# Performance work log

Hardware: AMD Instinct MI355X
Metric: run time of the kernel (lower is better)

## Reference

```python
import jax, jax.numpy as jnp
import numpy as np

NEG_BIG = -9e15
ALPHA = 0.2  # leakyrelu slope

N, IN_F, OUT_F = 8192, 512, 64


def setup_inputs() -> dict:
    key = jax.random.key(0)
    ks = jax.random.split(key, 7)
    return {
        "input": jax.random.normal(ks[0], (N, IN_F), dtype=jnp.float32),
        "W": jax.random.normal(ks[1], (IN_F, OUT_F), dtype=jnp.float32) * 0.05,
        "a": jax.random.normal(ks[2], (2 * OUT_F, 1), dtype=jnp.float32) * 0.1,
        "W_si": jax.random.normal(ks[3], (1, 1), dtype=jnp.float32),
        "W_ei": jax.random.normal(ks[4], (1, 1), dtype=jnp.float32),
        "adj_ad": jax.random.uniform(ks[5], (N, N), dtype=jnp.float32),
        "adj": jax.random.randint(ks[6], (N, N), 0, 2, dtype=jnp.int32),
    }


def reference(input, W, a, W_si, W_ei, adj_ad, adj):
    h = input @ W                                   # [N, F]
    F_ = h.shape[1]
    a1, a2 = a[:F_, 0], a[F_:, 0]                   # split concat projection
    # concat-score: a^T [h_i || h_j] == (h@a1)_i + (h@a2)_j, no [N,N,2F] tensor
    e = jax.nn.leaky_relu(h @ a1[:, None] + (h @ a2[:, None]).T, ALPHA)  # [N, N]
    e = jnp.abs(W_ei) * e + jnp.abs(W_si) * adj_ad
    attention = jnp.where(adj > 0, e, jnp.float32(NEG_BIG))
    attention = jax.nn.softmax(attention, axis=1)
    # dropout is identity in eval mode (training=False)
    h_prime = attention @ h                         # [N, F]
    return jax.nn.elu(h_prime)
```

## Files before the change

kernel.cpp:

```cpp
#include <hip/hip_runtime.h>
#include <math.h>

#define N 8192
#define IN_F 512
#define OUTF 64
#define TI 16
#define JT 256
#define NTILE (N / JT)
#define PS 264

typedef _Float16 f16x8 __attribute__((ext_vector_type(8)));
typedef float f32x4 __attribute__((ext_vector_type(4)));

#define OFF_HT   0u
#define OFF_S    262144u
#define OFF_T    270336u
#define OFF_TMAX 278528u

#define SB0() __builtin_amdgcn_sched_barrier(0)
#define SYNC()                                           \
  SB0();                                                 \
  asm volatile("s_waitcnt lgkmcnt(0)" ::: "memory");     \
  SB0();                                                 \
  __builtin_amdgcn_s_barrier();                          \
  SB0();

__device__ __forceinline__ unsigned enc_f32(float f) {
  unsigned b = __float_as_uint(f);
  return b ^ ((unsigned)((int)b >> 31) | 0x80000000u);
}

__global__ __launch_bounds__(64) void k_precompute(
    const float* __restrict__ input, const float* __restrict__ W,
    const float* __restrict__ a, const float* __restrict__ W_ei,
    _Float16* __restrict__ hT, float* __restrict__ s2,
    float* __restrict__ t2) {
  const int lane = threadIdx.x;
  const int i0 = blockIdx.x * 4;
  const float aei = fabsf(W_ei[0]);

  float acc[4] = {0.f, 0.f, 0.f, 0.f};
  for (int c = 0; c < IN_F; c += 4) {
    const float w0 = W[(c + 0) * OUTF + lane];
    const float w1 = W[(c + 1) * OUTF + lane];
    const float w2 = W[(c + 2) * OUTF + lane];
    const float w3 = W[(c + 3) * OUTF + lane];
    #pragma unroll
    for (int r = 0; r < 4; r++) {
      const float4 iv = *(const float4*)(input + (size_t)(i0 + r) * IN_F + c);
      acc[r] += iv.x * w0 + iv.y * w1 + iv.z * w2 + iv.w * w3;
    }
  }

  union { _Float16 f[4]; uint2 u; } pk;
  #pragma unroll
  for (int r = 0; r < 4; r++) pk.f[r] = (_Float16)acc[r];
  *(uint2*)(hT + (size_t)lane * N + i0) = pk.u;

  const float a1v = a[lane];
  const float a2v = a[OUTF + lane];
  #pragma unroll
  for (int r = 0; r < 4; r++) {
    float sv = acc[r] * a1v;
    float tv = acc[r] * a2v;
    #pragma unroll
    for (int off = 1; off < 64; off <<= 1) {
      sv += __shfl_xor(sv, off);
      tv += __shfl_xor(tv, off);
    }
    if (lane == 0) {
      s2[i0 + r] = aei * sv;
      t2[i0 + r] = aei * tv;
    }
  }
}

__global__ __launch_bounds__(512) void k_tmax(const float* __restrict__ t,
                                              unsigned* __restrict__ tmax) {
  __shared__ float red[8];
  const int tid = threadIdx.x;
  float m = t[blockIdx.x * 512 + tid];
  #pragma unroll
  for (int off = 1; off < 64; off <<= 1) m = fmaxf(m, __shfl_xor(m, off));
  if ((tid & 63) == 0) red[tid >> 6] = m;
  __syncthreads();
  if (tid == 0) {
    #pragma unroll
    for (int w = 1; w < 8; w++) m = fmaxf(m, red[w]);
    atomicMax(tmax, enc_f32(m));
  }
}

__global__ __launch_bounds__(512, 4) void k_attn(
    const _Float16* __restrict__ hT, const float* __restrict__ s2,
    const float* __restrict__ t2, const unsigned* __restrict__ tmaxp,
    const float* __restrict__ W_si, const float* __restrict__ W_ei,
    const float* __restrict__ adj_ad, const int* __restrict__ adj,
    float* __restrict__ out) {
  __shared__ __align__(16) float smem[8224];
  _Float16* P = (_Float16*)smem;

  const int tid = threadIdx.x;
  const int w = tid >> 6;
  const int lane = tid & 63;
  const int q = lane >> 4;
  const int m = lane & 15;
  const int h2 = lane >> 5;
  const int cw = lane & 31;
  const int i0 = blockIdx.x * TI;

  const float asi = fabsf(W_si[0]);
  (void)W_ei;
  const unsigned te = *tmaxp;
  const float tm2 = __uint_as_float((te & 0x80000000u) ? (te ^ 0x80000000u) : ~te);

  const int myrow = 2 * w + h2;
  const float s2r = s2[i0 + myrow];
  const float ym = s2r + tm2;
  const float MrB = fmaxf(ym, 0.2f * ym) + asi;

  float S = 0.f;
  f32x4 acc[4];
  #pragma unroll
  for (int nb = 0; nb < 4; nb++) acc[nb] = (f32x4){0.f, 0.f, 0.f, 0.f};

  const size_t gRow = (size_t)(i0 + myrow) * N;
  const int c0 = cw * 4;

  struct PF { float4 a0, a1; int4 k0, k1; };

  auto LOADT = [&](int kt) -> PF {
    const size_t b = gRow + (size_t)kt * JT + c0;
    PF p;
    p.a0 = *(const float4*)(adj_ad + b);
    p.a1 = *(const float4*)(adj_ad + b + 128);
    p.k0 = *(const int4*)(adj + b);
    p.k1 = *(const int4*)(adj + b + 128);
    return p;
  };

  auto EXPW = [&](int kt, const PF& p, const float4& tva, const float4& tvb) {
    const float ad[8] = {p.a0.x, p.a0.y, p.a0.z, p.a0.w,
                         p.a1.x, p.a1.y, p.a1.z, p.a1.w};
    const int mk[8] = {p.k0.x, p.k0.y, p.k0.z, p.k0.w,
                       p.k1.x, p.k1.y, p.k1.z, p.k1.w};
    const float tv[8] = {tva.x, tva.y, tva.z, tva.w,
                         tvb.x, tvb.y, tvb.z, tvb.w};
    union { _Float16 hh[8]; uint2 u[2]; } pk;
    #pragma unroll
    for (int e = 0; e < 8; e++) {
      const float y = s2r + tv[e];
      const float lr = fmaxf(y, 0.2f * y);
      const float arg = fmaf(asi, ad[e], lr - MrB);
      const float pv = __expf(arg) * (float)mk[e];
      S += pv;
      pk.hh[e] = (_Float16)pv;
    }
    _Float16* dst = P + (kt & 1) * (16 * PS) + myrow * PS;
    *(uint2*)(dst + c0) = pk.u[0];
    *(uint2*)(dst + c0 + 128) = pk.u[1];
  };

  #define MLOAD(kt, FB, FA)                                                   \
    {                                                                         \
      const int cb_ = (kt) * JT + w * 32 + q * 8;                             \
      _Pragma("unroll") for (int nb = 0; nb < 4; nb++)                        \
          FB[nb] = *(const f16x8*)(hT + (size_t)(nb * 16 + m) * N + cb_);     \
      FA = *(const f16x8*)(P + ((kt) & 1) * (16 * PS) + m * PS + w * 32 +     \
                           q * 8);                                            \
    }

  #define MSTEP(FB, FA)                                                       \
    {                                                                         \
      _Pragma("unroll") for (int nb = 0; nb < 4; nb++)                        \
          acc[nb] = __builtin_amdgcn_mfma_f32_16x16x32_f16(FA, FB[nb],        \
                                                           acc[nb], 0, 0, 0);\
    }

  PF pA = LOADT(0);
  PF pB;

  #pragma unroll 1
  for (int k = 0; k < NTILE; k += 2) {
    {
      const float4 tva = *(const float4*)(t2 + k * JT + c0);
      const float4 tvb = *(const float4*)(t2 + k * JT + c0 + 128);
      f16x8 fb[4], fa;
      if (k >= 1) MLOAD(k - 1, fb, fa);
      SB0();
      pB = LOADT(k + 1);
      SB0();
      if (k >= 1) MSTEP(fb, fa);
      EXPW(k, pA, tva, tvb);
      SYNC();
    }
    {
      const float4 tva = *(const float4*)(t2 + (k + 1) * JT + c0);
      const float4 tvb = *(const float4*)(t2 + (k + 1) * JT + c0 + 128);
      f16x8 fb[4], fa;
      MLOAD(k, fb, fa);
      SB0();
      if (k + 2 < NTILE) pA = LOADT(k + 2);
      SB0();
      MSTEP(fb, fa);
      EXPW(k + 1, pB, tva, tvb);
      SYNC();
    }
  }

  {
    f16x8 fb[4], fa;
    MLOAD(NTILE - 1, fb, fa);
    MSTEP(fb, fa);
  }

  #pragma unroll
  for (int off = 1; off < 32; off <<= 1) S += __shfl_xor(S, off);

  SYNC();

  if ((lane & 31) == 0) smem[8192 + myrow] = S;
  #pragma unroll
  for (int nb = 0; nb < 4; nb++) {
    #pragma unroll
    for (int reg = 0; reg < 4; reg++) {
      smem[w * 1024 + (q * 4 + reg) * 64 + nb * 16 + m] = acc[nb][reg];
    }
  }
  __syncthreads();

  #pragma unroll
  for (int ii = 0; ii < 2; ii++) {
    const int e = tid + 512 * ii;
    const int r = e >> 6;
    const int f = e & 63;
    float num = 0.f;
    #pragma unroll
    for (int ww = 0; ww < 8; ww++) num += smem[ww * 1024 + r * 64 + f];
    const float den = smem[8192 + r];
    const float x = num / den;
    out[(size_t)(i0 + r) * OUTF + f] = x > 0.f ? x : expm1f(x);
  }
}

extern "C" void kernel_launch(void* const* d_in, const int* in_sizes, int n_in,
                              void* d_out, int out_size, void* d_ws, size_t ws_size,
                              hipStream_t stream) {
  const float* input  = (const float*)d_in[0];
  const float* W      = (const float*)d_in[1];
  const float* a      = (const float*)d_in[2];
  const float* W_si   = (const float*)d_in[3];
  const float* W_ei   = (const float*)d_in[4];
  const float* adj_ad = (const float*)d_in[5];
  const int*   adj    = (const int*)d_in[6];
  float* out = (float*)d_out;
  float* ws  = (float*)d_ws;

  _Float16* hT   = (_Float16*)(ws + OFF_HT);
  float* s2      = ws + OFF_S;
  float* t2      = ws + OFF_T;
  unsigned* tmax = (unsigned*)(ws + OFF_TMAX);

  hipMemsetAsync(tmax, 0, 4, stream);
  k_precompute<<<N / 4, 64, 0, stream>>>(input, W, a, W_ei, hT, s2, t2);
  k_tmax<<<N / 512, 512, 0, stream>>>(t2, tmax);
  k_attn<<<N / TI, 512, 0, stream>>>(hT, s2, t2, tmax, W_si, W_ei,
                                     adj_ad, adj, out);
}
```

Baseline: 578.4 us.

## Pack adjacency into bitmask in precompute kernel and fuse tmax reduction

The precompute kernel now streams the int32 adjacency matrix once and packs it into a one-bit-per-entry mask. The attention kernel then reads a single mask byte per 8 columns instead of two int4 loads, which cuts its load pressure and register use. The separate tmax kernel is folded into precompute through a per-block atomicMax. The per-lane column mapping changes to 8 contiguous columns so the P tile is written with one 16-byte store. Total adj traffic is unchanged but moves into the small, lightly occupied precompute kernel, with an extra 8MB mask written and read back.

```diff
diff --git a/kernel.cpp b/kernel.cpp
--- a/kernel.cpp
+++ b/kernel.cpp
@@ -8,14 +8,17 @@
 #define JT 256
 #define NTILE (N / JT)
 #define PS 264
+#define MROW 1024
 
 typedef _Float16 f16x8 __attribute__((ext_vector_type(8)));
 typedef float f32x4 __attribute__((ext_vector_type(4)));
+typedef int i32x4 __attribute__((ext_vector_type(4)));
 
 #define OFF_HT   0u
 #define OFF_S    262144u
 #define OFF_T    270336u
 #define OFF_TMAX 278528u
+#define OFF_MASK 294912u
 
 #define SB0() __builtin_amdgcn_sched_barrier(0)
 #define SYNC()                                           \
@@ -33,70 +36,91 @@
 __global__ __launch_bounds__(64) void k_precompute(
     const float* __restrict__ input, const float* __restrict__ W,
     const float* __restrict__ a, const float* __restrict__ W_ei,
-    _Float16* __restrict__ hT, float* __restrict__ s2,
-    float* __restrict__ t2) {
+    const int* __restrict__ adj, _Float16* __restrict__ hT,
+    float* __restrict__ s2, float* __restrict__ t2,
+    unsigned* __restrict__ tmax, unsigned char* __restrict__ mask) {
   const int lane = threadIdx.x;
   const int i0 = blockIdx.x * 4;
   const float aei = fabsf(W_ei[0]);
 
-  float acc[4] = {0.f, 0.f, 0.f, 0.f};
-  for (int c = 0; c < IN_F; c += 4) {
-    const float w0 = W[(c + 0) * OUTF + lane];
-    const float w1 = W[(c + 1) * OUTF + lane];
-    const float w2 = W[(c + 2) * OUTF + lane];
-    const float w3 = W[(c + 3) * OUTF + lane];
+  auto GEMM = [&]() {
+    float acc[4] = {0.f, 0.f, 0.f, 0.f};
+    for (int c = 0; c < IN_F; c += 4) {
+      const float w0 = W[(c + 0) * OUTF + lane];
+      const float w1 = W[(c + 1) * OUTF + lane];
+      const float w2 = W[(c + 2) * OUTF + lane];
+      const float w3 = W[(c + 3) * OUTF + lane];
+      #pragma unroll
+      for (int r = 0; r < 4; r++) {
+        const float4 iv = *(const float4*)(input + (size_t)(i0 + r) * IN_F + c);
+        acc[r] += iv.x * w0 + iv.y * w1 + iv.z * w2 + iv.w * w3;
+      }
+    }
+
+    union { _Float16 f[4]; uint2 u; } pk;
+    #pragma unroll
+    for (int r = 0; r < 4; r++) pk.f[r] = (_Float16)acc[r];
+    *(uint2*)(hT + (size_t)lane * N + i0) = pk.u;
+
+    const float a1v = a[lane];
+    const float a2v = a[OUTF + lane];
+    float tloc = -1e30f;
     #pragma unroll
     for (int r = 0; r < 4; r++) {
-      const float4 iv = *(const float4*)(input + (size_t)(i0 + r) * IN_F + c);
-      acc[r] += iv.x * w0 + iv.y * w1 + iv.z * w2 + iv.w * w3;
-    }
-  }
-
-  union { _Float16 f[4]; uint2 u; } pk;
-  #pragma unroll
-  for (int r = 0; r < 4; r++) pk.f[r] = (_Float16)acc[r];
-  *(uint2*)(hT + (size_t)lane * N + i0) = pk.u;
-
-  const float a1v = a[lane];
-  const float a2v = a[OUTF + lane];
-  #pragma unroll
-  for (int r = 0; r < 4; r++) {
-    float sv = acc[r] * a1v;
-    float tv = acc[r] * a2v;
-    #pragma unroll
-    for (int off = 1; off < 64; off <<= 1) {
-      sv += __shfl_xor(sv, off);
-      tv += __shfl_xor(tv, off);
-    }
-    if (lane == 0) {
-      s2[i0 + r] = aei * sv;
-      t2[i0 + r] = aei * tv;
-    }
-  }
-}
-
-__global__ __launch_bounds__(512) void k_tmax(const float* __restrict__ t,
-                                              unsigned* __restrict__ tmax) {
-  __shared__ float red[8];
-  const int tid = threadIdx.x;
-  float m = t[blockIdx.x * 512 + tid];
-  #pragma unroll
-  for (int off = 1; off < 64; off <<= 1) m = fmaxf(m, __shfl_xor(m, off));
-  if ((tid & 63) == 0) red[tid >> 6] = m;
-  __syncthreads();
-  if (tid == 0) {
-    #pragma unroll
-    for (int w = 1; w < 8; w++) m = fmaxf(m, red[w]);
-    atomicMax(tmax, enc_f32(m));
-  }
+      float sv = acc[r] * a1v;
+      float tv = acc[r] * a2v;
+      #pragma unroll
+      for (int off = 1; off < 64; off <<= 1) {
+        sv += __shfl_xor(sv, off);
+        tv += __shfl_xor(tv, off);
+      }
+      if (lane == 0) {
+        s2[i0 + r] = aei * sv;
+        const float t2v = aei * tv;
+        t2[i0 + r] = t2v;
+        tloc = fmaxf(tloc, t2v);
+      }
+    }
+    if (lane == 0) atomicMax(tmax, enc_f32(tloc));
+  };
+
+  auto MASK = [&]() {
+    const unsigned gtid = blockIdx.x * 64 + lane;
+    #pragma unroll 1
+    for (int o = 0; o < 64; o += 4) {
+      i32x4 v[4][2];
+      #pragma unroll
+      for (int u = 0; u < 4; u++) {
+        const size_t B = gtid + (size_t)(o + u) * 131072;
+        const i32x4* p = (const i32x4*)adj + B * 2;
+        v[u][0] = __builtin_nontemporal_load(p);
+        v[u][1] = __builtin_nontemporal_load(p + 1);
+      }
+      #pragma unroll
+      for (int u = 0; u < 4; u++) {
+        const size_t B = gtid + (size_t)(o + u) * 131072;
+        const unsigned b = (unsigned)(v[u][0].x > 0) |
+                           ((unsigned)(v[u][0].y > 0) << 1) |
+                           ((unsigned)(v[u][0].z > 0) << 2) |
+                           ((unsigned)(v[u][0].w > 0) << 3) |
+                           ((unsigned)(v[u][1].x > 0) << 4) |
+                           ((unsigned)(v[u][1].y > 0) << 5) |
+                           ((unsigned)(v[u][1].z > 0) << 6) |
+                           ((unsigned)(v[u][1].w > 0) << 7);
+        mask[B] = (unsigned char)b;
+      }
+    }
+  };
+
+  if (blockIdx.x & 1) { MASK(); GEMM(); }
+  else                { GEMM(); MASK(); }
 }
 
 __global__ __launch_bounds__(512, 4) void k_attn(
     const _Float16* __restrict__ hT, const float* __restrict__ s2,
     const float* __restrict__ t2, const unsigned* __restrict__ tmaxp,
-    const float* __restrict__ W_si, const float* __restrict__ W_ei,
-    const float* __restrict__ adj_ad, const int* __restrict__ adj,
-    float* __restrict__ out) {
+    const float* __restrict__ W_si, const unsigned char* __restrict__ mask,
+    const float* __restrict__ adj_ad, float* __restrict__ out) {
   __shared__ __align__(16) float smem[8224];
   _Float16* P = (_Float16*)smem;
 
@@ -110,7 +134,6 @@
   const int i0 = blockIdx.x * TI;
 
   const float asi = fabsf(W_si[0]);
-  (void)W_ei;
   const unsigned te = *tmaxp;
   const float tm2 = __uint_as_float((te & 0x80000000u) ? (te ^ 0x80000000u) : ~te);
 
@@ -125,40 +148,37 @@
   for (int nb = 0; nb < 4; nb++) acc[nb] = (f32x4){0.f, 0.f, 0.f, 0.f};
 
   const size_t gRow = (size_t)(i0 + myrow) * N;
-  const int c0 = cw * 4;
-
-  struct PF { float4 a0, a1; int4 k0, k1; };
+  const unsigned char* mrow = mask + (size_t)(i0 + myrow) * MROW;
+  const int c0 = cw * 8;
+
+  struct PF { float4 a0, a1; unsigned mb; };
 
   auto LOADT = [&](int kt) -> PF {
     const size_t b = gRow + (size_t)kt * JT + c0;
     PF p;
     p.a0 = *(const float4*)(adj_ad + b);
-    p.a1 = *(const float4*)(adj_ad + b + 128);
-    p.k0 = *(const int4*)(adj + b);
-    p.k1 = *(const int4*)(adj + b + 128);
+    p.a1 = *(const float4*)(adj_ad + b + 4);
+    p.mb = mrow[kt * 32 + cw];
     return p;
   };
 
   auto EXPW = [&](int kt, const PF& p, const float4& tva, const float4& tvb) {
     const float ad[8] = {p.a0.x, p.a0.y, p.a0.z, p.a0.w,
                          p.a1.x, p.a1.y, p.a1.z, p.a1.w};
-    const int mk[8] = {p.k0.x, p.k0.y, p.k0.z, p.k0.w,
-                       p.k1.x, p.k1.y, p.k1.z, p.k1.w};
     const float tv[8] = {tva.x, tva.y, tva.z, tva.w,
                          tvb.x, tvb.y, tvb.z, tvb.w};
-    union { _Float16 hh[8]; uint2 u[2]; } pk;
+    union { _Float16 hh[8]; uint4 u4; } pk;
     #pragma unroll
     for (int e = 0; e < 8; e++) {
       const float y = s2r + tv[e];
       const float lr = fmaxf(y, 0.2f * y);
       const float arg = fmaf(asi, ad[e], lr - MrB);
-      const float pv = __expf(arg) * (float)mk[e];
+      const float pv = ((p.mb >> e) & 1u) ? __expf(arg) : 0.f;
       S += pv;
       pk.hh[e] = (_Float16)pv;
     }
     _Float16* dst = P + (kt & 1) * (16 * PS) + myrow * PS;
-    *(uint2*)(dst + c0) = pk.u[0];
-    *(uint2*)(dst + c0 + 128) = pk.u[1];
+    *(uint4*)(dst + c0) = pk.u4;
   };
 
   #define MLOAD(kt, FB, FA)                                                   \
@@ -184,7 +204,7 @@
   for (int k = 0; k < NTILE; k += 2) {
     {
       const float4 tva = *(const float4*)(t2 + k * JT + c0);
-      const float4 tvb = *(const float4*)(t2 + k * JT + c0 + 128);
+      const float4 tvb = *(const float4*)(t2 + k * JT + c0 + 4);
       f16x8 fb[4], fa;
       if (k >= 1) MLOAD(k - 1, fb, fa);
       SB0();
@@ -196,7 +216,7 @@
     }
     {
       const float4 tva = *(const float4*)(t2 + (k + 1) * JT + c0);
-      const float4 tvb = *(const float4*)(t2 + (k + 1) * JT + c0 + 128);
+      const float4 tvb = *(const float4*)(t2 + (k + 1) * JT + c0 + 4);
       f16x8 fb[4], fa;
       MLOAD(k, fb, fa);
       SB0();
@@ -256,14 +276,15 @@
   float* out = (float*)d_out;
   float* ws  = (float*)d_ws;
 
-  _Float16* hT   = (_Float16*)(ws + OFF_HT);
-  float* s2      = ws + OFF_S;
-  float* t2      = ws + OFF_T;
-  unsigned* tmax = (unsigned*)(ws + OFF_TMAX);
+  _Float16* hT        = (_Float16*)(ws + OFF_HT);
+  float* s2           = ws + OFF_S;
+  float* t2           = ws + OFF_T;
+  unsigned* tmax      = (unsigned*)(ws + OFF_TMAX);
+  unsigned char* mask = (unsigned char*)(ws + OFF_MASK);
 
   hipMemsetAsync(tmax, 0, 4, stream);
-  k_precompute<<<N / 4, 64, 0, stream>>>(input, W, a, W_ei, hT, s2, t2);
-  k_tmax<<<N / 512, 512, 0, stream>>>(t2, tmax);
-  k_attn<<<N / TI, 512, 0, stream>>>(hT, s2, t2, tmax, W_si, W_ei,
-                                     adj_ad, adj, out);
-}
+  k_precompute<<<N / 4, 64, 0, stream>>>(input, W, a, W_ei, adj, hT, s2, t2,
+                                         tmax, mask);
+  k_attn<<<N / TI, 512, 0, stream>>>(hT, s2, t2, tmax, W_si, mask,
+                                     adj_ad, out);
+}
```

After: 588.2 us. Within noise of the previous version (+1.7%).

## Split attention over column chunks with single-wave blocks and a finish kernel

Applied to the files above, without the earlier changes.

Restructures the attention kernel so each single-wavefront block handles 16 rows over one eighth of the columns. This removes the cross-wave LDS barriers and the in-block reduction, and partial numerators and denominators go to workspace. A new finish kernel sums the partials and applies normalization and ELU. The tmax reduction is folded into the precompute kernel via an atomic, which drops one launch. The cost is more partial-result traffic, an extra kernel, and hT fragments reloaded from global memory per block.

```diff
diff --git a/kernel.cpp b/kernel.cpp
--- a/kernel.cpp
+++ b/kernel.cpp
@@ -5,9 +5,11 @@
 #define IN_F 512
 #define OUTF 64
 #define TI 16
-#define JT 256
-#define NTILE (N / JT)
-#define PS 264
+#define JSPLIT 8
+#define JCH (N / JSPLIT)
+#define JT 64
+#define NT (JCH / JT)
+#define PS 72
 
 typedef _Float16 f16x8 __attribute__((ext_vector_type(8)));
 typedef float f32x4 __attribute__((ext_vector_type(4)));
@@ -16,14 +18,10 @@
 #define OFF_S    262144u
 #define OFF_T    270336u
 #define OFF_TMAX 278528u
+#define OFF_DEN  294912u
+#define OFF_NUM  360448u
 
 #define SB0() __builtin_amdgcn_sched_barrier(0)
-#define SYNC()                                           \
-  SB0();                                                 \
-  asm volatile("s_waitcnt lgkmcnt(0)" ::: "memory");     \
-  SB0();                                                 \
-  __builtin_amdgcn_s_barrier();                          \
-  SB0();
 
 __device__ __forceinline__ unsigned enc_f32(float f) {
   unsigned b = __float_as_uint(f);
@@ -34,7 +32,7 @@
     const float* __restrict__ input, const float* __restrict__ W,
     const float* __restrict__ a, const float* __restrict__ W_ei,
     _Float16* __restrict__ hT, float* __restrict__ s2,
-    float* __restrict__ t2) {
+    float* __restrict__ t2, unsigned* __restrict__ tmax) {
   const int lane = threadIdx.x;
   const int i0 = blockIdx.x * 4;
   const float aei = fabsf(W_ei[0]);
@@ -59,6 +57,7 @@
 
   const float a1v = a[lane];
   const float a2v = a[OUTF + lane];
+  float tloc = -1e30f;
   #pragma unroll
   for (int r = 0; r < 4; r++) {
     float sv = acc[r] * a1v;
@@ -70,177 +69,160 @@
     }
     if (lane == 0) {
       s2[i0 + r] = aei * sv;
-      t2[i0 + r] = aei * tv;
-    }
-  }
-}
-
-__global__ __launch_bounds__(512) void k_tmax(const float* __restrict__ t,
-                                              unsigned* __restrict__ tmax) {
-  __shared__ float red[8];
-  const int tid = threadIdx.x;
-  float m = t[blockIdx.x * 512 + tid];
-  #pragma unroll
-  for (int off = 1; off < 64; off <<= 1) m = fmaxf(m, __shfl_xor(m, off));
-  if ((tid & 63) == 0) red[tid >> 6] = m;
-  __syncthreads();
-  if (tid == 0) {
-    #pragma unroll
-    for (int w = 1; w < 8; w++) m = fmaxf(m, red[w]);
-    atomicMax(tmax, enc_f32(m));
-  }
-}
-
-__global__ __launch_bounds__(512, 4) void k_attn(
+      const float t2v = aei * tv;
+      t2[i0 + r] = t2v;
+      tloc = fmaxf(tloc, t2v);
+    }
+  }
+  if (lane == 0) atomicMax(tmax, enc_f32(tloc));
+}
+
+__global__ __launch_bounds__(64, 3) void k_attn(
     const _Float16* __restrict__ hT, const float* __restrict__ s2,
     const float* __restrict__ t2, const unsigned* __restrict__ tmaxp,
-    const float* __restrict__ W_si, const float* __restrict__ W_ei,
+    const float* __restrict__ W_si,
     const float* __restrict__ adj_ad, const int* __restrict__ adj,
-    float* __restrict__ out) {
-  __shared__ __align__(16) float smem[8224];
-  _Float16* P = (_Float16*)smem;
-
-  const int tid = threadIdx.x;
-  const int w = tid >> 6;
-  const int lane = tid & 63;
-  const int q = lane >> 4;
-  const int m = lane & 15;
-  const int h2 = lane >> 5;
-  const int cw = lane & 31;
-  const int i0 = blockIdx.x * TI;
+    float* __restrict__ numP, float* __restrict__ denP) {
+  __shared__ __align__(16) _Float16 P0[TI * PS];
+  __shared__ __align__(16) _Float16 P1[TI * PS];
+
+  const int lane = threadIdx.x;
+  const int g = lane >> 4;
+  const int cl = lane & 15;
+  const int ib = blockIdx.x >> 3;
+  const int js = blockIdx.x & 7;
+  const int i0 = ib * TI;
+  const int jb0 = js * JCH;
 
   const float asi = fabsf(W_si[0]);
-  (void)W_ei;
   const unsigned te = *tmaxp;
   const float tm2 = __uint_as_float((te & 0x80000000u) ? (te ^ 0x80000000u) : ~te);
 
-  const int myrow = 2 * w + h2;
-  const float s2r = s2[i0 + myrow];
-  const float ym = s2r + tm2;
-  const float MrB = fmaxf(ym, 0.2f * ym) + asi;
-
-  float S = 0.f;
+  float s2r[4], MrB[4];
+  #pragma unroll
+  for (int u = 0; u < 4; u++) {
+    s2r[u] = s2[i0 + 4 * u + g];
+    const float ym = s2r[u] + tm2;
+    MrB[u] = fmaxf(ym, 0.2f * ym) + asi;
+  }
+
+  float S[4] = {0.f, 0.f, 0.f, 0.f};
   f32x4 acc[4];
   #pragma unroll
   for (int nb = 0; nb < 4; nb++) acc[nb] = (f32x4){0.f, 0.f, 0.f, 0.f};
 
-  const size_t gRow = (size_t)(i0 + myrow) * N;
-  const int c0 = cw * 4;
-
-  struct PF { float4 a0, a1; int4 k0, k1; };
-
-  auto LOADT = [&](int kt) -> PF {
-    const size_t b = gRow + (size_t)kt * JT + c0;
-    PF p;
-    p.a0 = *(const float4*)(adj_ad + b);
-    p.a1 = *(const float4*)(adj_ad + b + 128);
-    p.k0 = *(const int4*)(adj + b);
-    p.k1 = *(const int4*)(adj + b + 128);
-    return p;
-  };
-
-  auto EXPW = [&](int kt, const PF& p, const float4& tva, const float4& tvb) {
-    const float ad[8] = {p.a0.x, p.a0.y, p.a0.z, p.a0.w,
-                         p.a1.x, p.a1.y, p.a1.z, p.a1.w};
-    const int mk[8] = {p.k0.x, p.k0.y, p.k0.z, p.k0.w,
-                       p.k1.x, p.k1.y, p.k1.z, p.k1.w};
-    const float tv[8] = {tva.x, tva.y, tva.z, tva.w,
-                         tvb.x, tvb.y, tvb.z, tvb.w};
-    union { _Float16 hh[8]; uint2 u[2]; } pk;
-    #pragma unroll
-    for (int e = 0; e < 8; e++) {
-      const float y = s2r + tv[e];
-      const float lr = fmaxf(y, 0.2f * y);
-      const float arg = fmaf(asi, ad[e], lr - MrB);
-      const float pv = __expf(arg) * (float)mk[e];
-      S += pv;
-      pk.hh[e] = (_Float16)pv;
-    }
-    _Float16* dst = P + (kt & 1) * (16 * PS) + myrow * PS;
-    *(uint2*)(dst + c0) = pk.u[0];
-    *(uint2*)(dst + c0 + 128) = pk.u[1];
-  };
-
-  #define MLOAD(kt, FB, FA)                                                   \
-    {                                                                         \
-      const int cb_ = (kt) * JT + w * 32 + q * 8;                             \
-      _Pragma("unroll") for (int nb = 0; nb < 4; nb++)                        \
-          FB[nb] = *(const f16x8*)(hT + (size_t)(nb * 16 + m) * N + cb_);     \
-      FA = *(const f16x8*)(P + ((kt) & 1) * (16 * PS) + m * PS + w * 32 +     \
-                           q * 8);                                            \
-    }
-
-  #define MSTEP(FB, FA)                                                       \
-    {                                                                         \
-      _Pragma("unroll") for (int nb = 0; nb < 4; nb++)                        \
-          acc[nb] = __builtin_amdgcn_mfma_f32_16x16x32_f16(FA, FB[nb],        \
-                                                           acc[nb], 0, 0, 0);\
-    }
-
-  PF pA = LOADT(0);
-  PF pB;
+  float4 vaA[4], vaB[4];
+  int4 vkA[4], vkB[4];
+
+  #define LOADS(kt, va, vk)                                                   \
+    {                                                                         \
+      const int cb_ = jb0 + (kt) * JT + cl * 4;                               \
+      _Pragma("unroll") for (int u = 0; u < 4; u++) {                         \
+        const size_t a_ = (size_t)(i0 + 4 * u + g) * N + cb_;                 \
+        va[u] = *(const float4*)(adj_ad + a_);                                \
+        vk[u] = *(const int4*)(adj + a_);                                     \
+      }                                                                       \
+    }
+
+  #define FBLOAD(kt, fb, t2v)                                                 \
+    {                                                                         \
+      const int jb_ = jb0 + (kt) * JT;                                        \
+      t2v = *(const float4*)(t2 + jb_ + cl * 4);                              \
+      _Pragma("unroll") for (int ks = 0; ks < 2; ks++)                        \
+        _Pragma("unroll") for (int nb = 0; nb < 4; nb++)                      \
+            fb[ks][nb] = *(const f16x8*)(hT + (size_t)(nb * 16 + cl) * N +    \
+                                         jb_ + ks * 32 + g * 8);              \
+    }
+
+  #define EXPW(va, vk, t2v, Pd)                                               \
+    {                                                                         \
+      const float tv_[4] = {t2v.x, t2v.y, t2v.z, t2v.w};                      \
+      _Pragma("unroll") for (int u = 0; u < 4; u++) {                         \
+        const float ad_[4] = {va[u].x, va[u].y, va[u].z, va[u].w};            \
+        const int mk_[4] = {vk[u].x, vk[u].y, vk[u].z, vk[u].w};              \
+        union { _Float16 h[4]; uint2 u2; } pk_;                               \
+        _Pragma("unroll") for (int e2 = 0; e2 < 4; e2++) {                    \
+          const float y_ = s2r[u] + tv_[e2];                                  \
+          const float lr_ = fmaxf(y_, 0.2f * y_);                             \
+          const float arg_ = fmaf(asi, ad_[e2], lr_ - MrB[u]);      \
+          const float pv_ = (mk_[e2] > 0) ? __expf(arg_) : 0.f;               \
+          S[u] += pv_;                                                        \
+          pk_.h[e2] = (_Float16)pv_;                                          \
+        }                                                                     \
+        *(uint2*)(Pd + (4 * u + g) * PS + cl * 4) = pk_.u2;                   \
+      }                                                                       \
+    }
+
+  #define MFMA4(Ps, fb)                                                       \
+    {                                                                         \
+      _Pragma("unroll") for (int ks = 0; ks < 2; ks++) {                      \
+        const f16x8 fa_ = *(const f16x8*)(Ps + cl * PS + ks * 32 + g * 8);    \
+        _Pragma("unroll") for (int nb = 0; nb < 4; nb++)                      \
+            acc[nb] = __builtin_amdgcn_mfma_f32_16x16x32_f16(                 \
+                fa_, fb[ks][nb], acc[nb], 0, 0, 0);                           \
+      }                                                                       \
+    }
+
+  LOADS(0, vaA, vkA);
+  SB0();
 
   #pragma unroll 1
-  for (int k = 0; k < NTILE; k += 2) {
+  for (int it = 0; it < NT / 2; it++) {
+    const int kt = 2 * it;
     {
-      const float4 tva = *(const float4*)(t2 + k * JT + c0);
-      const float4 tvb = *(const float4*)(t2 + k * JT + c0 + 128);
-      f16x8 fb[4], fa;
-      if (k >= 1) MLOAD(k - 1, fb, fa);
-      SB0();
-      pB = LOADT(k + 1);
-      SB0();
-      if (k >= 1) MSTEP(fb, fa);
-      EXPW(k, pA, tva, tvb);
-      SYNC();
+      f16x8 fb[2][4];
+      float4 t2v;
+      FBLOAD(kt, fb, t2v);
+      SB0();
+      LOADS(kt + 1, vaB, vkB);
+      SB0();
+      EXPW(vaA, vkA, t2v, P0);
+      MFMA4(P0, fb);
     }
     {
-      const float4 tva = *(const float4*)(t2 + (k + 1) * JT + c0);
-      const float4 tvb = *(const float4*)(t2 + (k + 1) * JT + c0 + 128);
-      f16x8 fb[4], fa;
-      MLOAD(k, fb, fa);
-      SB0();
-      if (k + 2 < NTILE) pA = LOADT(k + 2);
-      SB0();
-      MSTEP(fb, fa);
-      EXPW(k + 1, pB, tva, tvb);
-      SYNC();
-    }
-  }
-
-  {
-    f16x8 fb[4], fa;
-    MLOAD(NTILE - 1, fb, fa);
-    MSTEP(fb, fa);
-  }
-
-  #pragma unroll
-  for (int off = 1; off < 32; off <<= 1) S += __shfl_xor(S, off);
-
-  SYNC();
-
-  if ((lane & 31) == 0) smem[8192 + myrow] = S;
+      f16x8 fb[2][4];
+      float4 t2v;
+      FBLOAD(kt + 1, fb, t2v);
+      SB0();
+      if (it + 1 < NT / 2) LOADS(kt + 2, vaA, vkA);
+      SB0();
+      EXPW(vaB, vkB, t2v, P1);
+      MFMA4(P1, fb);
+    }
+  }
+
+  #pragma unroll
+  for (int u = 0; u < 4; u++) {
+    #pragma unroll
+    for (int off = 1; off < 16; off <<= 1) S[u] += __shfl_xor(S[u], off);
+  }
+  if (cl == 0) {
+    #pragma unroll
+    for (int u = 0; u < 4; u++) denP[js * N + i0 + 4 * u + g] = S[u];
+  }
   #pragma unroll
   for (int nb = 0; nb < 4; nb++) {
     #pragma unroll
     for (int reg = 0; reg < 4; reg++) {
-      smem[w * 1024 + (q * 4 + reg) * 64 + nb * 16 + m] = acc[nb][reg];
-    }
-  }
-  __syncthreads();
-
-  #pragma unroll
-  for (int ii = 0; ii < 2; ii++) {
-    const int e = tid + 512 * ii;
-    const int r = e >> 6;
-    const int f = e & 63;
-    float num = 0.f;
-    #pragma unroll
-    for (int ww = 0; ww < 8; ww++) num += smem[ww * 1024 + r * 64 + f];
-    const float den = smem[8192 + r];
-    const float x = num / den;
-    out[(size_t)(i0 + r) * OUTF + f] = x > 0.f ? x : expm1f(x);
-  }
+      numP[((size_t)js * N + i0 + g * 4 + reg) * OUTF + nb * 16 + cl] =
+          acc[nb][reg];
+    }
+  }
+}
+
+__global__ __launch_bounds__(256) void k_finish(
+    const float* __restrict__ numP, const float* __restrict__ denP,
+    float* __restrict__ out) {
+  const int e = blockIdx.x * 256 + threadIdx.x;
+  const int i = e >> 6;
+  float num = 0.f, den = 0.f;
+  #pragma unroll
+  for (int js = 0; js < JSPLIT; js++) {
+    num += numP[(size_t)js * (N * OUTF) + e];
+    den += denP[js * N + i];
+  }
+  const float x = num / den;
+  out[e] = x > 0.f ? x : expm1f(x);
 }
 
 extern "C" void kernel_launch(void* const* d_in, const int* in_sizes, int n_in,
@@ -260,10 +242,12 @@
   float* s2      = ws + OFF_S;
   float* t2      = ws + OFF_T;
   unsigned* tmax = (unsigned*)(ws + OFF_TMAX);
+  float* denP    = ws + OFF_DEN;
+  float* numP    = ws + OFF_NUM;
 
   hipMemsetAsync(tmax, 0, 4, stream);
-  k_precompute<<<N / 4, 64, 0, stream>>>(input, W, a, W_ei, hT, s2, t2);
-  k_tmax<<<N / 512, 512, 0, stream>>>(t2, tmax);
-  k_attn<<<N / TI, 512, 0, stream>>>(hT, s2, t2, tmax, W_si, W_ei,
-                                     adj_ad, adj, out);
-}
+  k_precompute<<<N / 4, 64, 0, stream>>>(input, W, a, W_ei, hT, s2, t2, tmax);
+  k_attn<<<(N / TI) * JSPLIT, 64, 0, stream>>>(hT, s2, t2, tmax, W_si,
+                                               adj_ad, adj, numP, denP);
+  k_finish<<<N * OUTF / 256, 256, 0, stream>>>(numP, denP, out);
+}
```

Result: slower. 636.5 us (+10.0%).
